# Kernel optimization log

Hardware: AMD Instinct MI355X
Metric: run time of the kernel (lower is better)

## Reference

```python
import jax, jax.numpy as jnp
import numpy as np

EPS = 1e-30


def _logmmexp(P, logW):
    """Stable logsumexp_k(P[..., k] + logW[a, k]) -> (..., a) via max-shifted matmul."""
    mP = jnp.max(P, axis=-1, keepdims=True)          # (..., 1)
    mW = jnp.max(logW, axis=-1, keepdims=True)       # (A, 1)
    out = jnp.einsum('...k,ak->...a', jnp.exp(P - mP), jnp.exp(logW - mW))
    return jnp.log(out) + mP + mW[:, 0]


def _inside_chart(tokens, log_binary, log_lexical):
    B, L = tokens.shape
    N = log_binary.shape[0]
    chart = jnp.full((B, N, L, L + 1), -jnp.inf, dtype=log_lexical.dtype)
    # Base case: chart[:, :, i, i+1] = log_lexical[:, tokens[:, i]]
    lex = jnp.transpose(log_lexical[:, tokens], (1, 0, 2))  # (B, N, L)
    ii = jnp.arange(L)
    chart = chart.at[:, :, ii, ii + 1].set(lex)
    # CKY recursion: loop over span length (structural, static), vectorize over
    # start positions i and split points k.
    for s in range(2, L + 1):
        pos = L - s + 1
        i = np.arange(pos)
        m = np.arange(s - 1)
        k_idx = i[:, None] + m[None, :] + 1                 # (pos, s-1) split points
        left = chart[:, :, i[:, None], k_idx]               # (B, N, pos, s-1)
        right = chart[:, :, k_idx, (i + s)[:, None]]        # (B, N, pos, s-1)
        lt = jnp.transpose(left, (0, 2, 3, 1))              # (B, pos, m, N_B)
        rt = jnp.transpose(right, (0, 2, 3, 1))             # (B, pos, m, N_C)
        # P[b,i,m,B,C] = left + right
        P = lt[..., :, None] + rt[..., None, :]             # (B, pos, m, N, N)
        Pf = P.reshape(B, pos, (s - 1) * N * N)
        logW = jnp.broadcast_to(log_binary[:, None, :, :], (N, s - 1, N, N)).reshape(N, -1)
        scores = _logmmexp(Pf, logW)                        # (B, pos, N_A)
        chart = chart.at[:, :, i, i + s].set(jnp.transpose(scores, (0, 2, 1)))
    return chart


def setup_inputs() -> dict:
    key = jax.random.key(0)
    k1, k2, k3 = jax.random.split(key, 3)
    B, L, N, T = 32, 32, 48, 32000
    tokens = jax.random.randint(k1, (B, L), 0, T)
    binary = jax.random.uniform(k2, (N, N, N), dtype=jnp.float32)
    lexical = jax.random.uniform(k3, (N, T), dtype=jnp.float32)
    return {"tokens": tokens, "binary": binary, "lexical": lexical}


def reference(tokens, binary, lexical):
    start = 0
    log_binary = jnp.log(jnp.clip(binary, EPS))
    log_lexical = jnp.log(jnp.clip(lexical, EPS))
    chart = _inside_chart(tokens, log_binary, log_lexical)
    return chart[:, start, 0, tokens.shape[1]]  # (B,) sentence log-probs
```

## Files before the change

### kernel.cpp

```cpp
#include <hip/hip_runtime.h>
#include <math.h>

#define NNT 48
#define LL 32
#define BB 32
#define N2 2304
#define KSTEPS 72
#define EPSV 1e-30f
#define CH_J ((LL+1)*NNT)
#define SEB_S 2328
#define PD_RS 20
#define PD_T  328
#define PD_W  984
#define NCELL (BB*LL*(LL+1)*NNT)

typedef __attribute__((ext_vector_type(8))) short bf16x8;
typedef __attribute__((ext_vector_type(4))) float f32x4;
typedef __attribute__((ext_vector_type(4))) int   i32x4;

__device__ __forceinline__ int ch_idx(int b, int i, int j, int n) {
    return (((b*LL + i)*(LL+1) + j)*NNT + n);
}
__device__ __forceinline__ unsigned short f2bf(float x) {
    unsigned u = __float_as_uint(x);
    u = (u + 0x7fffu + ((u >> 16) & 1u)) >> 16;
    return (unsigned short)u;
}
__device__ __forceinline__ int cvtpk(float lo, float hi) {
    int r;
    asm("v_cvt_pk_bf16_f32 %0, %1, %2" : "=v"(r) : "v"(lo), "v"(hi));
    return r;
}
__device__ __forceinline__ int uvt_base(int q, int r, int kc) {
    return q*1536 + ((((r << 2) + kc) ^ (r & 7)) << 3);
}
__device__ __forceinline__ float wavemax(float x) {
    #pragma unroll
    for (int o = 32; o; o >>= 1) x = fmaxf(x, __shfl_xor(x, o));
    return x;
}
__device__ __forceinline__ float ch_ld(const float* p) {
    return __hip_atomic_load(p, __ATOMIC_RELAXED, __HIP_MEMORY_SCOPE_AGENT);
}
__device__ __forceinline__ void ch_st(float* p, float v) {
    __hip_atomic_store(p, v, __ATOMIC_RELAXED, __HIP_MEMORY_SCOPE_AGENT);
}
#define LBAR() { asm volatile("s_waitcnt lgkmcnt(0)" ::: "memory"); \
                 __builtin_amdgcn_s_barrier(); }

__global__ void prep_kernel(const float* __restrict__ binary, const int* __restrict__ tokens,
                            const float* __restrict__ lexical, unsigned short* __restrict__ Wp,
                            float* __restrict__ chart, int T) {
    if (blockIdx.x < 432) {
        int idx = blockIdx.x*256 + threadIdx.x;
        int j  = idx & 7;
        int l  = (idx >> 3) & 63;
        int ks = (idx >> 9) % KSTEPS;
        int nt = idx / (KSTEPS*512);
        int e = ks*32 + ((l >> 4) << 3) + j;
        int n = nt*16 + (l & 15);
        int bp = e % 48, c = e / 48;
        Wp[idx] = f2bf(fmaxf(binary[n*N2 + bp*48 + c], EPSV));
    } else if (blockIdx.x < 688) {
        int row = (blockIdx.x - 432)*4 + (threadIdx.x >> 6);
        int lane = threadIdx.x & 63;
        int b = row >> 5, i = row & 31;
        int tok = tokens[b*LL + i];
        float val = (lane < NNT)
            ? __logf(fmaxf(lexical[(size_t)lane*(size_t)T + (size_t)tok], EPSV))
            : -INFINITY;
        float rm = wavemax(val);
        if (lane < NNT) chart[ch_idx(b, i, i+1, lane)] = val;
        if (lane == 0) chart[ch_idx(b, i, 0, i+1)] = rm;
    } else {
        int idx = (blockIdx.x - 688)*256 + threadIdx.x;
        if (idx < NCELL) {
            int n = idx % NNT;
            int r = idx / NNT;
            int j = r % (LL + 1);
            int i = (r / (LL + 1)) % LL;
            if (j != i + 1 && !(j == 0 && n == i + 1))
                chart[idx] = -INFINITY;
        }
    }
}

#define MFMA16(A,B,C) __builtin_amdgcn_mfma_f32_16x16x32_bf16(A,B,C,0,0,0)

#define LDVP(V, C, TCX, VPX)                                                   \
    { _Pragma("unroll")                                                        \
      for (int dt = 0; dt < 8; ++dt) {                                         \
          int t = (C)*8 + dt; int tt = (t < (TCX)) ? t : (TCX) - 1;            \
          int kk = rr + tt*2;                                                  \
          V[dt] = ch_ld((VPX) + kk*CH_J + ln);                                 \
      } }
#define FRESHFIX(V)                                                            \
    { if (freshLDS) {                                                          \
          if (lane == 0) btP = sRm[q + 1][s - 1];                              \
          if (rr == 0) V[0] = sOut[q + 1][ln];                                 \
      } }
#define CONSCH(V, C)                                                           \
    { int pv[4];                                                               \
      _Pragma("unroll")                                                        \
      for (int dp = 0; dp < 4; ++dp) {                                         \
          int t0 = (C)*8 + 2*dp;                                               \
          int tt0 = (t0     < tc) ? t0     : tc - 1;                           \
          int tt1 = (t0 + 1 < tc) ? t0 + 1 : tc - 1;                           \
          float a0 = sRm[q][rr + tt0*2 + 1];                                   \
          float a1 = sRm[q][rr + tt1*2 + 1];                                   \
          float e0 = __expf(V[2*dp]     + a0 - M);                             \
          float e1 = __expf(V[2*dp + 1] + a1 - M);                             \
          pv[dp] = cvtpk(e0, e1);                                              \
      }                                                                        \
      if (lane < NNT) {                                                        \
          int ad = uvt_base(w, lane, (C));                                     \
          *(i32x4*)&sUV[ad + 12288] = (i32x4){pv[0],pv[1],pv[2],pv[3]};        \
      } }

__global__ __launch_bounds__(512, 2) void inside_kernel(
        const unsigned short* __restrict__ Wp,
        float* __restrict__ chart,
        float* __restrict__ out) {
    const int pb = blockIdx.x;
    const int b = pb & 31, c = pb >> 5;
    const int i_base = 28 - 4*c;
    const int tid = threadIdx.x, lane = tid & 63, w = tid >> 6;
    const int fr = lane & 15, kg = lane >> 4;
    const int ln = (lane < NNT) ? lane : 0;
    const int q = w >> 1, rr = w & 1;
    const int i0 = i_base + q;

    __shared__ __align__(16) short sUV[24576];
    __shared__ __align__(16) short sEb[16*SEB_S];
    __shared__ float pD[8*PD_W];
    __shared__ float sRm[4][33];
    __shared__ float sOut[4][NNT];

    for (int x = tid; x < 12288; x += 512) ((int*)sUV)[x] = 0;
    for (int x = tid; x < 18624; x += 512) ((int*)sEb)[x] = 0;
    if (tid < 4)
        sRm[tid][1] = ch_ld(&chart[ch_idx(b, i_base + tid, 0, i_base + tid + 1)]);
    if (w < 4 && lane < NNT)
        sOut[w][lane] = ch_ld(&chart[ch_idx(b, i_base + w, i_base + w + 1, lane)]);

    const bf16x8* wp8 = (const bf16x8*)Wp;
    const int kstart = 9*w;
    bf16x8 wreg[9][3];
    #pragma unroll
    for (int t = 0; t < 9; ++t)
        #pragma unroll
        for (int nt = 0; nt < 3; ++nt)
            wreg[t][nt] = wp8[(nt*KSTEPS + kstart + t)*64 + lane];

    float vvP0[8] = {0,0,0,0,0,0,0,0}, vvP1[8] = {0,0,0,0,0,0,0,0}, btP = 0.f;
    if (i0 <= LL - 2) {
        const int nkn = 1, tcn = (nkn - rr + 1) >> 1;
        if (tcn > 0) {
            const float* vpn = chart + ch_idx(b, i0 + 1, i0 + 2, 0);
            const float* bpn = chart + ch_idx(b, i0 + 1, 0, i0 + 2);
            btP = (lane < nkn) ? ch_ld(bpn + lane*CH_J) : 0.f;
            LDVP(vvP0, 0, tcn, vpn)
        }
    }

    __syncthreads();

    for (int s = 2; s <= LL; ++s) {
        const int nk = s - 1;
        if (i_base > LL - s) return;

        const bool active = (i0 <= LL - s);
        const int tc = active ? ((nk - rr + 1) >> 1) : 0;
        const bool freshLDS = active && (s > 2) && (q < 3);
        float M = -INFINITY;
        f32x4 ea[9];
        #pragma unroll
        for (int z = 0; z < 9; ++z) ea[z] = (f32x4){0.f, 0.f, 0.f, 0.f};

        if (active && rr == ((nk - 1) & 1) && lane < NNT) {
            int tn = (nk - 1 - rr) >> 1;
            float eu = __expf(sOut[q][lane] - sRm[q][s - 1]);
            sUV[uvt_base(w, lane, tn >> 3) + (tn & 7)] = (short)f2bf(eu);
        }

        if (tc > 0) {
            const float* vp = chart + ch_idx(b, i0 + 1, i0 + s, 0);
            const float* bp = chart + ch_idx(b, i0 + 1, 0, i0 + s);

            FRESHFIX(vvP0)
            if (q == 3 && s > 2) {
                if (lane == 0) btP = ch_ld(bp);
                if (rr == 0)  vvP0[0] = ch_ld(vp + ln);
            }
            for (;;) {
                bool bad = (lane < nk) && (btP == -INFINITY);
                #pragma unroll
                for (int dt = 0; dt < 8; ++dt) bad |= (vvP0[dt] == -INFINITY);
                if (tc > 8) {
                    #pragma unroll
                    for (int dt = 0; dt < 8; ++dt) bad |= (vvP1[dt] == -INFINITY);
                }
                if (!__any(bad)) break;
                btP = (lane < nk) ? ch_ld(bp + lane*CH_J) : 0.f;
                LDVP(vvP0, 0, tc, vp)
                if (tc > 8) { LDVP(vvP1, 1, tc, vp) }
                FRESHFIX(vvP0)
            }

            {
                float al = (lane < nk) ? sRm[q][lane + 1] : -INFINITY;
                M = wavemax((lane < nk) ? al + btP : -INFINITY);
            }

            CONSCH(vvP0, 0)
            if (tc > 8) { CONSCH(vvP1, 1) }

            bf16x8 A0 = *(const bf16x8*)&sUV[uvt_base(w,  0 + fr, kg)];
            bf16x8 A1 = *(const bf16x8*)&sUV[uvt_base(w, 16 + fr, kg)];
            bf16x8 A2 = *(const bf16x8*)&sUV[uvt_base(w, 32 + fr, kg)];
            bf16x8 B0 = *(const bf16x8*)&sUV[12288 + uvt_base(w,  0 + fr, kg)];
            bf16x8 B1 = *(const bf16x8*)&sUV[12288 + uvt_base(w, 16 + fr, kg)];
            bf16x8 B2 = *(const bf16x8*)&sUV[12288 + uvt_base(w, 32 + fr, kg)];
            ea[0] = MFMA16(A0,B0,ea[0]); ea[1] = MFMA16(A0,B1,ea[1]); ea[2] = MFMA16(A0,B2,ea[2]);
            ea[3] = MFMA16(A1,B0,ea[3]); ea[4] = MFMA16(A1,B1,ea[4]); ea[5] = MFMA16(A1,B2,ea[5]);
            ea[6] = MFMA16(A2,B0,ea[6]); ea[7] = MFMA16(A2,B1,ea[7]); ea[8] = MFMA16(A2,B2,ea[8]);
        }

        if (s < LL && i0 <= LL - s - 1) {
            const int nkn = s;
            const int tcn = (nkn - rr + 1) >> 1;
            const float* vpn = chart + ch_idx(b, i0 + 1, i0 + s + 1, 0);
            const float* bpn = chart + ch_idx(b, i0 + 1, 0, i0 + s + 1);
            btP = (lane < nkn) ? ch_ld(bpn + lane*CH_J) : 0.f;
            LDVP(vvP0, 0, tcn, vpn)
            if (tcn > 8) { LDVP(vvP1, 1, tcn, vpn) }
        }

        if (active) {
            #pragma unroll
            for (int mt = 0; mt < 3; ++mt) {
                #pragma unroll
                for (int ct = 0; ct < 3; ++ct) {
                    f32x4 d = ea[mt*3 + ct];
                    int e0 = (ct*16 + fr)*48 + mt*16 + kg*4;
                    unsigned lo = (unsigned)cvtpk(d[0], d[1]);
                    unsigned hi = (unsigned)cvtpk(d[2], d[3]);
                    *(unsigned long long*)&sEb[w*SEB_S + e0] =
                        (unsigned long long)lo | ((unsigned long long)hi << 32);
                }
            }
        }

        LBAR();

        {
            f32x4 c0 = {0.f,0.f,0.f,0.f}, c1 = c0, c2 = c0;
            #pragma unroll
            for (int t = 0; t < 9; ++t) {
                bf16x8 af = *(const bf16x8*)&sEb[fr*SEB_S + (kstart + t)*32 + kg*8];
                c0 = MFMA16(af, wreg[t][0], c0);
                c1 = MFMA16(af, wreg[t][1], c1);
                c2 = MFMA16(af, wreg[t][2], c2);
            }
            #pragma unroll
            for (int r2 = 0; r2 < 4; ++r2) {
                int row = kg*4 + r2;
                pD[w*PD_W + 0*PD_T + row*PD_RS + fr] = c0[r2];
                pD[w*PD_W + 1*PD_T + row*PD_RS + fr] = c1[r2];
                pD[w*PD_W + 2*PD_T + row*PD_RS + fr] = c2[r2];
            }
        }
        LBAR();

        if (active && rr == 0) {
            float sum = 0.f;
            #pragma unroll
            for (int w2 = 0; w2 < 8; ++w2) {
                const float* pp = &pD[w2*PD_W + (ln >> 4)*PD_T + (ln & 15)];
                sum += pp[(2*q)*PD_RS] + pp[(2*q + 1)*PD_RS];
            }
            float val = M + __logf(sum);
            float rm = wavemax((lane < NNT) ? val : -INFINITY);
            if (lane < NNT) {
                ch_st(&chart[ch_idx(b, i0, i0 + s, lane)], val);
                sOut[q][lane] = val;
            }
            if (lane == 0) {
                ch_st(&chart[ch_idx(b, i0, 0, i0 + s)], rm);
                sRm[q][s] = rm;
                if (s == LL) out[b] = val;
            }
        }
        LBAR();
    }
}

extern "C" void kernel_launch(void* const* d_in, const int* in_sizes, int n_in,
                              void* d_out, int out_size, void* d_ws, size_t ws_size,
                              hipStream_t stream) {
    const int*   tokens  = (const int*)d_in[0];
    const float* binary  = (const float*)d_in[1];
    const float* lexical = (const float*)d_in[2];
    float* out = (float*)d_out;

    float* chart = (float*)d_ws;
    unsigned short* Wp = (unsigned short*)(chart + (size_t)NCELL);

    int T = in_sizes[2] / NNT;

    int fill_blocks = (NCELL + 255)/256;
    prep_kernel<<<688 + fill_blocks, 256, 0, stream>>>(binary, tokens, lexical, Wp, chart, T);
    inside_kernel<<<256, 512, 0, stream>>>(Wp, chart, out);
}
```

Baseline: 118.4 us.

## Use 1024-thread blocks covering eight start positions with streamed binary weights

Each block now handles eight start positions per sentence with 16 waves, halving the grid to 128 blocks of 1024 threads. Binary-rule weights are no longer held in registers; each wave streams its uneven K-slice from global memory every span step. The per-wave partial results go through shared memory as packed bf16 instead of fp32 to fit LDS, and the U/V staging buffers are folded into the existing sEb buffer. This is meant to share more of the chart work per block and reduce inter-block chart polling, at the cost of repeated global weight loads, fewer blocks on the device and lower precision in the partial sums.

```diff
diff --git a/kernel.cpp b/kernel.cpp
--- a/kernel.cpp
+++ b/kernel.cpp
@@ -9,9 +9,8 @@
 #define EPSV 1e-30f
 #define CH_J ((LL+1)*NNT)
 #define SEB_S 2328
-#define PD_RS 20
-#define PD_T  328
-#define PD_W  984
+#define PDC 20
+#define PD_W (3*16*PDC)
 #define NCELL (BB*LL*(LL+1)*NNT)
 
 typedef __attribute__((ext_vector_type(8))) short bf16x8;
@@ -31,8 +30,8 @@
     asm("v_cvt_pk_bf16_f32 %0, %1, %2" : "=v"(r) : "v"(lo), "v"(hi));
     return r;
 }
-__device__ __forceinline__ int uvt_base(int q, int r, int kc) {
-    return q*1536 + ((((r << 2) + kc) ^ (r & 7)) << 3);
+__device__ __forceinline__ int evo(int r, int kc) {
+    return (((r << 2) + kc) ^ (r & 7)) << 3;
 }
 __device__ __forceinline__ float wavemax(float x) {
     #pragma unroll
@@ -113,44 +112,39 @@
           pv[dp] = cvtpk(e0, e1);                                              \
       }                                                                        \
       if (lane < NNT) {                                                        \
-          int ad = uvt_base(w, lane, (C));                                     \
-          *(i32x4*)&sUV[ad + 12288] = (i32x4){pv[0],pv[1],pv[2],pv[3]};        \
+          int ad = w*SEB_S + evo(lane, (C));                                   \
+          *(i32x4*)&sEb[ad] = (i32x4){pv[0],pv[1],pv[2],pv[3]};                \
       } }
 
-__global__ __launch_bounds__(512, 2) void inside_kernel(
+__global__ __launch_bounds__(1024) void inside_kernel(
         const unsigned short* __restrict__ Wp,
         float* __restrict__ chart,
         float* __restrict__ out) {
     const int pb = blockIdx.x;
     const int b = pb & 31, c = pb >> 5;
-    const int i_base = 28 - 4*c;
+    const int i_base = 24 - 8*c;
     const int tid = threadIdx.x, lane = tid & 63, w = tid >> 6;
     const int fr = lane & 15, kg = lane >> 4;
     const int ln = (lane < NNT) ? lane : 0;
     const int q = w >> 1, rr = w & 1;
     const int i0 = i_base + q;
 
-    __shared__ __align__(16) short sUV[24576];
+    __shared__ __align__(16) short sEU[16*1536];
     __shared__ __align__(16) short sEb[16*SEB_S];
-    __shared__ float pD[8*PD_W];
-    __shared__ float sRm[4][33];
-    __shared__ float sOut[4][NNT];
-
-    for (int x = tid; x < 12288; x += 512) ((int*)sUV)[x] = 0;
-    for (int x = tid; x < 18624; x += 512) ((int*)sEb)[x] = 0;
-    if (tid < 4)
+    __shared__ __align__(8) unsigned short sPD[16*PD_W];
+    __shared__ float sRm[8][33];
+    __shared__ float sOut[8][NNT];
+
+    for (int x = tid; x < 12288; x += 1024) ((int*)sEU)[x] = 0;
+    for (int x = tid; x < 18624; x += 1024) ((int*)sEb)[x] = 0;
+    if (tid < 8)
         sRm[tid][1] = ch_ld(&chart[ch_idx(b, i_base + tid, 0, i_base + tid + 1)]);
-    if (w < 4 && lane < NNT)
+    if (w < 8 && lane < NNT)
         sOut[w][lane] = ch_ld(&chart[ch_idx(b, i_base + w, i_base + w + 1, lane)]);
 
     const bf16x8* wp8 = (const bf16x8*)Wp;
-    const int kstart = 9*w;
-    bf16x8 wreg[9][3];
-    #pragma unroll
-    for (int t = 0; t < 9; ++t)
-        #pragma unroll
-        for (int nt = 0; nt < 3; ++nt)
-            wreg[t][nt] = wp8[(nt*KSTEPS + kstart + t)*64 + lane];
+    const int kstart = (w < 8) ? 5*w : 40 + 4*(w - 8);
+    const int kcnt   = (w < 8) ? 5 : 4;
 
     float vvP0[8] = {0,0,0,0,0,0,0,0}, vvP1[8] = {0,0,0,0,0,0,0,0}, btP = 0.f;
     if (i0 <= LL - 2) {
@@ -171,7 +165,7 @@
 
         const bool active = (i0 <= LL - s);
         const int tc = active ? ((nk - rr + 1) >> 1) : 0;
-        const bool freshLDS = active && (s > 2) && (q < 3);
+        const bool freshLDS = active && (s > 2) && (q < 7);
         float M = -INFINITY;
         f32x4 ea[9];
         #pragma unroll
@@ -180,7 +174,7 @@
         if (active && rr == ((nk - 1) & 1) && lane < NNT) {
             int tn = (nk - 1 - rr) >> 1;
             float eu = __expf(sOut[q][lane] - sRm[q][s - 1]);
-            sUV[uvt_base(w, lane, tn >> 3) + (tn & 7)] = (short)f2bf(eu);
+            sEU[w*1536 + evo(lane, tn >> 3) + (tn & 7)] = (short)f2bf(eu);
         }
 
         if (tc > 0) {
@@ -188,7 +182,7 @@
             const float* bp = chart + ch_idx(b, i0 + 1, 0, i0 + s);
 
             FRESHFIX(vvP0)
-            if (q == 3 && s > 2) {
+            if (q == 7 && s > 2) {
                 if (lane == 0) btP = ch_ld(bp);
                 if (rr == 0)  vvP0[0] = ch_ld(vp + ln);
             }
@@ -215,12 +209,12 @@
             CONSCH(vvP0, 0)
             if (tc > 8) { CONSCH(vvP1, 1) }
 
-            bf16x8 A0 = *(const bf16x8*)&sUV[uvt_base(w,  0 + fr, kg)];
-            bf16x8 A1 = *(const bf16x8*)&sUV[uvt_base(w, 16 + fr, kg)];
-            bf16x8 A2 = *(const bf16x8*)&sUV[uvt_base(w, 32 + fr, kg)];
-            bf16x8 B0 = *(const bf16x8*)&sUV[12288 + uvt_base(w,  0 + fr, kg)];
-            bf16x8 B1 = *(const bf16x8*)&sUV[12288 + uvt_base(w, 16 + fr, kg)];
-            bf16x8 B2 = *(const bf16x8*)&sUV[12288 + uvt_base(w, 32 + fr, kg)];
+            bf16x8 A0 = *(const bf16x8*)&sEU[w*1536 + evo( 0 + fr, kg)];
+            bf16x8 A1 = *(const bf16x8*)&sEU[w*1536 + evo(16 + fr, kg)];
+            bf16x8 A2 = *(const bf16x8*)&sEU[w*1536 + evo(32 + fr, kg)];
+            bf16x8 B0 = *(const bf16x8*)&sEb[w*SEB_S + evo( 0 + fr, kg)];
+            bf16x8 B1 = *(const bf16x8*)&sEb[w*SEB_S + evo(16 + fr, kg)];
+            bf16x8 B2 = *(const bf16x8*)&sEb[w*SEB_S + evo(32 + fr, kg)];
             ea[0] = MFMA16(A0,B0,ea[0]); ea[1] = MFMA16(A0,B1,ea[1]); ea[2] = MFMA16(A0,B2,ea[2]);
             ea[3] = MFMA16(A1,B0,ea[3]); ea[4] = MFMA16(A1,B1,ea[4]); ea[5] = MFMA16(A1,B2,ea[5]);
             ea[6] = MFMA16(A2,B0,ea[6]); ea[7] = MFMA16(A2,B1,ea[7]); ea[8] = MFMA16(A2,B2,ea[8]);
@@ -255,29 +249,36 @@
 
         {
             f32x4 c0 = {0.f,0.f,0.f,0.f}, c1 = c0, c2 = c0;
-            #pragma unroll
-            for (int t = 0; t < 9; ++t) {
-                bf16x8 af = *(const bf16x8*)&sEb[fr*SEB_S + (kstart + t)*32 + kg*8];
-                c0 = MFMA16(af, wreg[t][0], c0);
-                c1 = MFMA16(af, wreg[t][1], c1);
-                c2 = MFMA16(af, wreg[t][2], c2);
-            }
-            #pragma unroll
-            for (int r2 = 0; r2 < 4; ++r2) {
-                int row = kg*4 + r2;
-                pD[w*PD_W + 0*PD_T + row*PD_RS + fr] = c0[r2];
-                pD[w*PD_W + 1*PD_T + row*PD_RS + fr] = c1[r2];
-                pD[w*PD_W + 2*PD_T + row*PD_RS + fr] = c2[r2];
-            }
+            for (int t = 0; t < kcnt; ++t) {
+                int ks = kstart + t;
+                bf16x8 af = *(const bf16x8*)&sEb[fr*SEB_S + ks*32 + kg*8];
+                bf16x8 q0 = wp8[(0*KSTEPS + ks)*64 + lane];
+                bf16x8 q1 = wp8[(1*KSTEPS + ks)*64 + lane];
+                bf16x8 q2 = wp8[(2*KSTEPS + ks)*64 + lane];
+                c0 = MFMA16(af, q0, c0);
+                c1 = MFMA16(af, q1, c1);
+                c2 = MFMA16(af, q2, c2);
+            }
+            unsigned l0 = (unsigned)cvtpk(c0[0], c0[1]), h0 = (unsigned)cvtpk(c0[2], c0[3]);
+            unsigned l1 = (unsigned)cvtpk(c1[0], c1[1]), h1 = (unsigned)cvtpk(c1[2], c1[3]);
+            unsigned l2 = (unsigned)cvtpk(c2[0], c2[1]), h2 = (unsigned)cvtpk(c2[2], c2[3]);
+            *(unsigned long long*)&sPD[((w*3 + 0)*16 + fr)*PDC + kg*4] =
+                (unsigned long long)l0 | ((unsigned long long)h0 << 32);
+            *(unsigned long long*)&sPD[((w*3 + 1)*16 + fr)*PDC + kg*4] =
+                (unsigned long long)l1 | ((unsigned long long)h1 << 32);
+            *(unsigned long long*)&sPD[((w*3 + 2)*16 + fr)*PDC + kg*4] =
+                (unsigned long long)l2 | ((unsigned long long)h2 << 32);
         }
         LBAR();
 
         if (active && rr == 0) {
+            const int nt = ln >> 4, colI = ln & 15;
             float sum = 0.f;
             #pragma unroll
-            for (int w2 = 0; w2 < 8; ++w2) {
-                const float* pp = &pD[w2*PD_W + (ln >> 4)*PD_T + (ln & 15)];
-                sum += pp[(2*q)*PD_RS] + pp[(2*q + 1)*PD_RS];
+            for (int w2 = 0; w2 < 16; ++w2) {
+                unsigned uu = *(const unsigned*)&sPD[((w2*3 + nt)*16 + colI)*PDC + 2*q];
+                sum += __uint_as_float((uu & 0xffffu) << 16)
+                     + __uint_as_float(uu & 0xffff0000u);
             }
             float val = M + __logf(sum);
             float rm = wavemax((lane < NNT) ? val : -INFINITY);
@@ -310,5 +311,5 @@
 
     int fill_blocks = (NCELL + 255)/256;
     prep_kernel<<<688 + fill_blocks, 256, 0, stream>>>(binary, tokens, lexical, Wp, chart, T);
-    inside_kernel<<<256, 512, 0, stream>>>(Wp, chart, out);
-}
+    inside_kernel<<<128, 1024, 0, stream>>>(Wp, chart, out);
+}
```

Measured after the change: 192.9 us. 62.9% more time.
